# Kernel tuning notes

Measured on AMD Instinct MI355X. Metric: run time of the kernel, lower is better.

The kernel has to match this reference:

```python
import jax, jax.numpy as jnp
import numpy as np

DIM = 1024
NUM_HEADS = 16
HEAD_DIM = DIM // NUM_HEADS
B, S = 2, 2048


def setup_inputs() -> dict:
    key = jax.random.key(0)
    ks = jax.random.split(key, 7)
    x = jax.random.normal(ks[0], (B, S, DIM), dtype=jnp.float32)
    cos = jax.random.uniform(ks[1], (S, HEAD_DIM // 2), dtype=jnp.float32)
    sin = jax.random.uniform(ks[2], (S, HEAD_DIM // 2), dtype=jnp.float32)
    scale = 1.0 / np.sqrt(DIM)
    Wq = jax.random.normal(ks[3], (DIM, DIM), dtype=jnp.float32) * scale
    Wk = jax.random.normal(ks[4], (DIM, DIM), dtype=jnp.float32) * scale
    Wv = jax.random.normal(ks[5], (DIM, DIM), dtype=jnp.float32) * scale
    Wo = jax.random.normal(ks[6], (DIM, DIM), dtype=jnp.float32) * scale
    return {"x": x, "cos": cos, "sin": sin, "Wq": Wq, "Wk": Wk, "Wv": Wv, "Wo": Wo}


def _apply_rope(t, c, s):
    # t: [B, S, H, hd]; c, s: [1, S, 1, hd] (already doubled)
    half = t.shape[-1] // 2
    t1, t2 = t[..., :half], t[..., half:]
    rot = jnp.concatenate([-t2, t1], axis=-1)
    return t * c + rot * s


def reference(x, cos, sin, Wq, Wk, Wv, Wo):
    Bs, Ss, D = x.shape
    H, hd = NUM_HEADS, HEAD_DIM
    q = (x @ Wq).reshape(Bs, Ss, H, hd)
    k = (x @ Wk).reshape(Bs, Ss, H, hd)
    v = (x @ Wv).reshape(Bs, Ss, H, hd)
    # repeat(1,1,1,2) in torch tiles cos as [cos, cos] along last dim
    c = jnp.concatenate([cos, cos], axis=-1)[None, :, None, :]
    s = jnp.concatenate([sin, sin], axis=-1)[None, :, None, :]
    q = _apply_rope(q, c, s)
    k = _apply_rope(k, c, s)
    # SDPA, non-causal, scale 1/sqrt(hd)
    scores = jnp.einsum("bqhd,bkhd->bhqk", q, k) / jnp.sqrt(jnp.float32(hd))
    attn = jax.nn.softmax(scores, axis=-1)
    out = jnp.einsum("bhqk,bkhd->bqhd", attn, v).reshape(Bs, Ss, D)
    return out @ Wo
```

## Files before the change

### kernel.cpp

```cpp
#include <hip/hip_runtime.h>

#define B_  2
#define S_  2048
#define D_  1024
#define H_  16
#define HD_ 64
#define M_  (B_*S_)

typedef __bf16 bf16x8 __attribute__((ext_vector_type(8)));
typedef float  f32x4  __attribute__((ext_vector_type(4)));
typedef float  f32x16 __attribute__((ext_vector_type(16)));
typedef unsigned short ushort_t;

static __device__ __forceinline__ ushort_t f2bf(float f) {
  __bf16 b = (__bf16)f;
  return __builtin_bit_cast(ushort_t, b);
}

typedef __attribute__((address_space(1))) const unsigned u32g;
typedef __attribute__((address_space(3))) unsigned u32l;
static __device__ __forceinline__ void gll16(const ushort_t* g, __bf16* l) {
  __builtin_amdgcn_global_load_lds((u32g*)g, (u32l*)l, 16, 0, 0);
}

__global__ __launch_bounds__(256) void convert_x(const float* __restrict__ x,
                                                 ushort_t* __restrict__ xb) {
  size_t e = ((size_t)blockIdx.x * 256 + threadIdx.x) * 8;
  float4 a = *(const float4*)(x + e);
  float4 b = *(const float4*)(x + e + 4);
  uint4 pk;
  pk.x = (unsigned)f2bf(a.x) | ((unsigned)f2bf(a.y) << 16);
  pk.y = (unsigned)f2bf(a.z) | ((unsigned)f2bf(a.w) << 16);
  pk.z = (unsigned)f2bf(b.x) | ((unsigned)f2bf(b.y) << 16);
  pk.w = (unsigned)f2bf(b.z) | ((unsigned)f2bf(b.w) << 16);
  *(uint4*)(xb + e) = pk;
}

__global__ __launch_bounds__(256) void transpose_w(const float* __restrict__ Wq,
                                                   const float* __restrict__ Wk,
                                                   const float* __restrict__ Wv,
                                                   const float* __restrict__ Wo,
                                                   ushort_t* __restrict__ Wqkvt,
                                                   ushort_t* __restrict__ Wot) {
  __shared__ __bf16 T[64][72];
  const int z = blockIdx.z;
  const float* W = (z == 0) ? Wq : (z == 1) ? Wk : (z == 2) ? Wv : Wo;
  ushort_t* Wt = (z < 3) ? (Wqkvt + (size_t)z * 1048576) : Wot;
  const int k0 = blockIdx.y * 64, n0 = blockIdx.x * 64;
  const int t = threadIdx.x, r = t >> 2, c16 = (t & 3) * 16;
#pragma unroll
  for (int i = 0; i < 4; i++) {
    float4 v = *(const float4*)(W + (size_t)(k0 + r) * D_ + n0 + c16 + i * 4);
    T[r][c16 + i*4 + 0] = (__bf16)v.x;
    T[r][c16 + i*4 + 1] = (__bf16)v.y;
    T[r][c16 + i*4 + 2] = (__bf16)v.z;
    T[r][c16 + i*4 + 3] = (__bf16)v.w;
  }
  __syncthreads();
  ushort_t vals[16];
#pragma unroll
  for (int i = 0; i < 16; i++) vals[i] = __builtin_bit_cast(ushort_t, T[c16 + i][r]);
  ushort_t* dst = Wt + (size_t)(n0 + r) * D_ + k0 + c16;
  *(uint4*)dst       = *(const uint4*)&vals[0];
  *(uint4*)(dst + 8) = *(const uint4*)&vals[8];
}

__global__ __launch_bounds__(256) void transpose_v(const ushort_t* __restrict__ Vb,
                                                   ushort_t* __restrict__ Vtg) {
  __shared__ __bf16 T[64][72];
  const int bh = blockIdx.y, kt = blockIdx.x;
  const int t = threadIdx.x, r = t >> 2, c16 = (t & 3) * 16;
  const ushort_t* src = Vb + ((size_t)bh * S_ + kt*64 + r) * 64 + c16;
  *(uint4*)&T[r][c16]     = *(const uint4*)src;
  *(uint4*)&T[r][c16 + 8] = *(const uint4*)(src + 8);
  __syncthreads();
  ushort_t vals[16];
#pragma unroll
  for (int i = 0; i < 16; i++) {
    int c = c16 + i;
    int k = ((c & 1) << 5) | (c >> 1);
    vals[i] = __builtin_bit_cast(ushort_t, T[k][r]);
  }
  ushort_t* dst = Vtg + ((size_t)bh * 64 + r) * S_ + kt*64 + c16;
  *(uint4*)dst       = *(const uint4*)&vals[0];
  *(uint4*)(dst + 8) = *(const uint4*)&vals[8];
}

template<int OMODE>
__global__ __launch_bounds__(256) void gemm_bf16(const ushort_t* __restrict__ A,
                                                 const ushort_t* __restrict__ Bt,
                                                 void* __restrict__ Cp,
                                                 const float* __restrict__ cosb,
                                                 const float* __restrict__ sinb) {
  __shared__ __bf16 As[4096];
  __shared__ __bf16 Bs[4096];
  const int t = threadIdx.x, w = t >> 6, lane = t & 63, l15 = lane & 15, g = lane >> 4;
  const int wr = w >> 1, wc = w & 1;
  const int row0 = blockIdx.y * 128, col0 = blockIdx.x * 128;
  const int lr = t >> 2, lc = (t & 3) * 8;
  f32x4 acc[4][4] = {};

  for (int k0 = 0; k0 < D_; k0 += 32) {
    __syncthreads();
#pragma unroll
    for (int i = 0; i < 2; i++) {
      gll16(A  + (size_t)(row0 + i*64 + lr) * D_ + k0 + lc, &As[i*2048 + w*512]);
      gll16(Bt + (size_t)(col0 + i*64 + lr) * D_ + k0 + lc, &Bs[i*2048 + w*512]);
    }
    __syncthreads();
    bf16x8 af[4], bfv[4];
#pragma unroll
    for (int mt = 0; mt < 4; mt++) af[mt]  = *(const bf16x8*)&As[(wr*64 + mt*16 + l15)*32 + g*8];
#pragma unroll
    for (int nt = 0; nt < 4; nt++) bfv[nt] = *(const bf16x8*)&Bs[(wc*64 + nt*16 + l15)*32 + g*8];
#pragma unroll
    for (int mt = 0; mt < 4; mt++)
#pragma unroll
      for (int nt = 0; nt < 4; nt++)
        acc[mt][nt] = __builtin_amdgcn_mfma_f32_16x16x32_bf16(af[mt], bfv[nt], acc[mt][nt], 0, 0, 0);
  }

  if (OMODE == 0) {
#pragma unroll
    for (int mt = 0; mt < 4; mt++)
#pragma unroll
      for (int nt = 0; nt < 4; nt++) {
        int col = col0 + wc*64 + nt*16 + l15;
#pragma unroll
        for (int reg = 0; reg < 4; reg++) {
          int r = row0 + wr*64 + mt*16 + g*4 + reg;
          ((float*)Cp)[(size_t)r * D_ + col] = acc[mt][nt][reg];
        }
      }
  } else {
    const int mat = col0 >> 10;
    const int nc0 = (col0 + wc*64) & 1023;
    const int h = nc0 >> 6;
    ushort_t* dst = (ushort_t*)Cp + (size_t)mat * 4194304;
    const float QS = 0.125f * 1.4426950408889634f;
#pragma unroll
    for (int mt = 0; mt < 4; mt++) {
#pragma unroll
      for (int reg = 0; reg < 4; reg++) {
        int r = row0 + wr*64 + mt*16 + g*4 + reg;
        int b = r >> 11, s = r & (S_ - 1);
        size_t base = (((size_t)(b*H_ + h) * S_ + s) << 6);
        if (mat < 2) {
#pragma unroll
          for (int nt = 0; nt < 2; nt++) {
            int d1 = nt*16 + l15;
            float c  = cosb[s*32 + d1];
            float sn = sinb[s*32 + d1];
            float v1 = acc[mt][nt][reg], v2 = acc[mt][nt+2][reg];
            float r1 = v1*c - v2*sn;
            float r2 = v2*c + v1*sn;
            if (mat == 0) { r1 *= QS; r2 *= QS; }
            dst[base + d1]      = f2bf(r1);
            dst[base + d1 + 32] = f2bf(r2);
          }
        } else {
#pragma unroll
          for (int nt = 0; nt < 4; nt++)
            dst[base + nt*16 + l15] = f2bf(acc[mt][nt][reg]);
        }
      }
    }
  }
}

__global__ __launch_bounds__(256) void attn32(const ushort_t* __restrict__ Q,
                                              const ushort_t* __restrict__ K,
                                              const ushort_t* __restrict__ Vtg,
                                              ushort_t* __restrict__ Oa) {
  __shared__ __bf16 Ks[64][72];
  __shared__ __bf16 Vt[64][72];
  __shared__ __bf16 Ps[4][32][72];
  const int t = threadIdx.x, w = t >> 6, lane = t & 63;
  const int l31 = lane & 31, h2 = lane >> 5;
  const int bh = blockIdx.y, q0 = blockIdx.x * 128 + w * 32;

  const ushort_t* Qp = Q + ((size_t)bh * S_ + q0 + l31) * HD_;
  bf16x8 qf[4];
#pragma unroll
  for (int kc = 0; kc < 4; kc++) qf[kc] = *(const bf16x8*)(Qp + kc*16 + h2*8);

  f32x16 o0 = {}, o1 = {};
  float lp[16];
#pragma unroll
  for (int i = 0; i < 16; i++) lp[i] = 0.f;

  const ushort_t* Kb = K   + (size_t)bh * S_ * HD_;
  const ushort_t* Vg = Vtg + (size_t)bh * HD_ * S_;
  const int sr = t >> 3, sc8 = (t & 7) * 8;

  uint4 ka, kb, va, vb;
  {
    ka = *(const uint4*)(Kb + (size_t)(sr)      * HD_ + sc8);
    kb = *(const uint4*)(Kb + (size_t)(sr + 32) * HD_ + sc8);
    va = *(const uint4*)(Vg + (size_t)(sr)      * S_  + sc8);
    vb = *(const uint4*)(Vg + (size_t)(sr + 32) * S_  + sc8);
  }

  for (int kt = 0; kt < S_ / 64; kt++) {
    __syncthreads();
    *(uint4*)&Ks[sr][sc8]      = ka;
    *(uint4*)&Ks[sr + 32][sc8] = kb;
    *(uint4*)&Vt[sr][sc8]      = va;
    *(uint4*)&Vt[sr + 32][sc8] = vb;
    __syncthreads();
    if (kt < S_/64 - 1) {
      ka = *(const uint4*)(Kb + (size_t)((kt+1)*64 + sr)      * HD_ + sc8);
      kb = *(const uint4*)(Kb + (size_t)((kt+1)*64 + sr + 32) * HD_ + sc8);
      va = *(const uint4*)(Vg + (size_t)(sr)      * S_ + (kt+1)*64 + sc8);
      vb = *(const uint4*)(Vg + (size_t)(sr + 32) * S_ + (kt+1)*64 + sc8);
    }

    f32x16 s0 = {}, s1 = {};
#pragma unroll
    for (int kc = 0; kc < 4; kc++) {
      bf16x8 b0 = *(const bf16x8*)&Ks[l31][kc*16 + h2*8];
      bf16x8 b1 = *(const bf16x8*)&Ks[32 + l31][kc*16 + h2*8];
      s0 = __builtin_amdgcn_mfma_f32_32x32x16_bf16(qf[kc], b0, s0, 0, 0, 0);
      s1 = __builtin_amdgcn_mfma_f32_32x32x16_bf16(qf[kc], b1, s1, 0, 0, 0);
    }

#pragma unroll
    for (int i = 0; i < 16; i++) {
      float p0 = exp2f(s0[i]);
      float p1 = exp2f(s1[i]);
      lp[i] += p0 + p1;
      int row = (i & 3) + 8*(i >> 2) + 4*h2;
      unsigned pk = (unsigned)f2bf(p0) | ((unsigned)f2bf(p1) << 16);
      *(unsigned*)&Ps[w][row][2*l31] = pk;
    }

#pragma unroll
    for (int kc = 0; kc < 4; kc++) {
      bf16x8 pf = *(const bf16x8*)&Ps[w][l31][kc*16 + h2*8];
      bf16x8 v0 = *(const bf16x8*)&Vt[l31][kc*16 + h2*8];
      bf16x8 v1 = *(const bf16x8*)&Vt[32 + l31][kc*16 + h2*8];
      o0 = __builtin_amdgcn_mfma_f32_32x32x16_bf16(pf, v0, o0, 0, 0, 0);
      o1 = __builtin_amdgcn_mfma_f32_32x32x16_bf16(pf, v1, o1, 0, 0, 0);
    }
  }

#pragma unroll
  for (int i = 0; i < 16; i++) {
#pragma unroll
    for (int mk = 1; mk < 32; mk <<= 1) lp[i] += __shfl_xor(lp[i], mk, 64);
  }

  int b = bh >> 4, h = bh & 15;
#pragma unroll
  for (int i = 0; i < 16; i++) {
    float inv = 1.f / lp[i];
    int row = q0 + (i & 3) + 8*(i >> 2) + 4*h2;
    size_t base = (size_t)(b*S_ + row) * D_ + h*64;
    Oa[base + l31]      = f2bf(o0[i] * inv);
    Oa[base + 32 + l31] = f2bf(o1[i] * inv);
  }
}

extern "C" void kernel_launch(void* const* d_in, const int* in_sizes, int n_in,
                              void* d_out, int out_size, void* d_ws, size_t ws_size,
                              hipStream_t stream) {
  (void)in_sizes; (void)n_in; (void)out_size; (void)ws_size;
  const float* x    = (const float*)d_in[0];
  const float* cosb = (const float*)d_in[1];
  const float* sinb = (const float*)d_in[2];
  const float* Wq   = (const float*)d_in[3];
  const float* Wk   = (const float*)d_in[4];
  const float* Wv   = (const float*)d_in[5];
  const float* Wo   = (const float*)d_in[6];
  float* out = (float*)d_out;

  ushort_t* w     = (ushort_t*)d_ws;
  ushort_t* xb    = w;
  ushort_t* Wqkvt = w + 4194304;
  ushort_t* Wot   = w + 7340032;
  ushort_t* Qb    = w + 8388608;
  ushort_t* Kb    = w + 12582912;
  ushort_t* Vb    = w + 16777216;
  ushort_t* Vtg   = w + 20971520;
  ushort_t* att   = w + 25165824;

  convert_x<<<2048, 256, 0, stream>>>(x, xb);
  transpose_w<<<dim3(16, 16, 4), 256, 0, stream>>>(Wq, Wk, Wv, Wo, Wqkvt, Wot);

  gemm_bf16<1><<<dim3(24, 32), 256, 0, stream>>>(xb, Wqkvt, Qb, cosb, sinb);

  transpose_v<<<dim3(32, 32), 256, 0, stream>>>(Vb, Vtg);

  attn32<<<dim3(16, 32), 256, 0, stream>>>(Qb, Kb, Vtg, att);

  gemm_bf16<0><<<dim3(8, 32), 256, 0, stream>>>(att, Wot, out, nullptr, nullptr);
}
```

Before: 224.4 us.

## Split attention over key halves with combine pass; narrow output GEMM tiles

The attention kernel now splits the key/value sequence into two halves across a third grid dimension, writing unnormalized bf16 partial outputs and row sums into reused workspace buffers. A new combine kernel adds the partials and normalizes. The output projection GEMM is templated to a 64-wide N tile so it launches twice as many blocks. The aim is more blocks in flight to fill the GPU's compute units, at the cost of an extra kernel, extra memory traffic, and bf16 rounding of the partial sums. The split is only valid because the softmax has no max subtraction, so the two partials share a scale.

```diff
diff --git a/kernel.cpp b/kernel.cpp
--- a/kernel.cpp
+++ b/kernel.cpp
@@ -15,6 +15,9 @@
 static __device__ __forceinline__ ushort_t f2bf(float f) {
   __bf16 b = (__bf16)f;
   return __builtin_bit_cast(ushort_t, b);
+}
+static __device__ __forceinline__ float bf2f(ushort_t u) {
+  return (float)__builtin_bit_cast(__bf16, u);
 }
 
 typedef __attribute__((address_space(1))) const unsigned u32g;
@@ -86,37 +89,39 @@
   *(uint4*)(dst + 8) = *(const uint4*)&vals[8];
 }
 
-template<int OMODE>
+template<int OMODE, int BN>
 __global__ __launch_bounds__(256) void gemm_bf16(const ushort_t* __restrict__ A,
                                                  const ushort_t* __restrict__ Bt,
                                                  void* __restrict__ Cp,
                                                  const float* __restrict__ cosb,
                                                  const float* __restrict__ sinb) {
+  constexpr int NF = BN / 32;
   __shared__ __bf16 As[4096];
-  __shared__ __bf16 Bs[4096];
+  __shared__ __bf16 Bs[BN * 32];
   const int t = threadIdx.x, w = t >> 6, lane = t & 63, l15 = lane & 15, g = lane >> 4;
   const int wr = w >> 1, wc = w & 1;
-  const int row0 = blockIdx.y * 128, col0 = blockIdx.x * 128;
+  const int row0 = blockIdx.y * 128, col0 = blockIdx.x * BN;
   const int lr = t >> 2, lc = (t & 3) * 8;
-  f32x4 acc[4][4] = {};
+  f32x4 acc[4][NF] = {};
 
   for (int k0 = 0; k0 < D_; k0 += 32) {
     __syncthreads();
 #pragma unroll
-    for (int i = 0; i < 2; i++) {
-      gll16(A  + (size_t)(row0 + i*64 + lr) * D_ + k0 + lc, &As[i*2048 + w*512]);
+    for (int i = 0; i < 2; i++)
+      gll16(A + (size_t)(row0 + i*64 + lr) * D_ + k0 + lc, &As[i*2048 + w*512]);
+#pragma unroll
+    for (int i = 0; i < BN/64; i++)
       gll16(Bt + (size_t)(col0 + i*64 + lr) * D_ + k0 + lc, &Bs[i*2048 + w*512]);
-    }
     __syncthreads();
-    bf16x8 af[4], bfv[4];
-#pragma unroll
-    for (int mt = 0; mt < 4; mt++) af[mt]  = *(const bf16x8*)&As[(wr*64 + mt*16 + l15)*32 + g*8];
-#pragma unroll
-    for (int nt = 0; nt < 4; nt++) bfv[nt] = *(const bf16x8*)&Bs[(wc*64 + nt*16 + l15)*32 + g*8];
+    bf16x8 af[4], bfv[NF];
+#pragma unroll
+    for (int mt = 0; mt < 4; mt++)  af[mt]  = *(const bf16x8*)&As[(wr*64 + mt*16 + l15)*32 + g*8];
+#pragma unroll
+    for (int nt = 0; nt < NF; nt++) bfv[nt] = *(const bf16x8*)&Bs[(wc*(BN/2) + nt*16 + l15)*32 + g*8];
 #pragma unroll
     for (int mt = 0; mt < 4; mt++)
 #pragma unroll
-      for (int nt = 0; nt < 4; nt++)
+      for (int nt = 0; nt < NF; nt++)
         acc[mt][nt] = __builtin_amdgcn_mfma_f32_16x16x32_bf16(af[mt], bfv[nt], acc[mt][nt], 0, 0, 0);
   }
 
@@ -124,8 +129,8 @@
 #pragma unroll
     for (int mt = 0; mt < 4; mt++)
 #pragma unroll
-      for (int nt = 0; nt < 4; nt++) {
-        int col = col0 + wc*64 + nt*16 + l15;
+      for (int nt = 0; nt < NF; nt++) {
+        int col = col0 + wc*(BN/2) + nt*16 + l15;
 #pragma unroll
         for (int reg = 0; reg < 4; reg++) {
           int r = row0 + wr*64 + mt*16 + g*4 + reg;
@@ -171,13 +176,15 @@
 __global__ __launch_bounds__(256) void attn32(const ushort_t* __restrict__ Q,
                                               const ushort_t* __restrict__ K,
                                               const ushort_t* __restrict__ Vtg,
-                                              ushort_t* __restrict__ Oa) {
+                                              ushort_t* __restrict__ op0,
+                                              ushort_t* __restrict__ op1,
+                                              float* __restrict__ lw) {
   __shared__ __bf16 Ks[64][72];
   __shared__ __bf16 Vt[64][72];
   __shared__ __bf16 Ps[4][32][72];
   const int t = threadIdx.x, w = t >> 6, lane = t & 63;
   const int l31 = lane & 31, h2 = lane >> 5;
-  const int bh = blockIdx.y, q0 = blockIdx.x * 128 + w * 32;
+  const int bh = blockIdx.y, q0 = blockIdx.x * 128 + w * 32, z = blockIdx.z;
 
   const ushort_t* Qp = Q + ((size_t)bh * S_ + q0 + l31) * HD_;
   bf16x8 qf[4];
@@ -189,26 +196,24 @@
 #pragma unroll
   for (int i = 0; i < 16; i++) lp[i] = 0.f;
 
-  const ushort_t* Kb = K   + (size_t)bh * S_ * HD_;
-  const ushort_t* Vg = Vtg + (size_t)bh * HD_ * S_;
+  const ushort_t* Kb = K   + ((size_t)bh * S_ + z * 1024) * HD_;
+  const ushort_t* Vg = Vtg + (size_t)bh * HD_ * S_ + z * 1024;
   const int sr = t >> 3, sc8 = (t & 7) * 8;
 
   uint4 ka, kb, va, vb;
-  {
-    ka = *(const uint4*)(Kb + (size_t)(sr)      * HD_ + sc8);
-    kb = *(const uint4*)(Kb + (size_t)(sr + 32) * HD_ + sc8);
-    va = *(const uint4*)(Vg + (size_t)(sr)      * S_  + sc8);
-    vb = *(const uint4*)(Vg + (size_t)(sr + 32) * S_  + sc8);
-  }
-
-  for (int kt = 0; kt < S_ / 64; kt++) {
+  ka = *(const uint4*)(Kb + (size_t)(sr)      * HD_ + sc8);
+  kb = *(const uint4*)(Kb + (size_t)(sr + 32) * HD_ + sc8);
+  va = *(const uint4*)(Vg + (size_t)(sr)      * S_  + sc8);
+  vb = *(const uint4*)(Vg + (size_t)(sr + 32) * S_  + sc8);
+
+  for (int kt = 0; kt < 16; kt++) {
     __syncthreads();
     *(uint4*)&Ks[sr][sc8]      = ka;
     *(uint4*)&Ks[sr + 32][sc8] = kb;
     *(uint4*)&Vt[sr][sc8]      = va;
     *(uint4*)&Vt[sr + 32][sc8] = vb;
     __syncthreads();
-    if (kt < S_/64 - 1) {
+    if (kt < 15) {
       ka = *(const uint4*)(Kb + (size_t)((kt+1)*64 + sr)      * HD_ + sc8);
       kb = *(const uint4*)(Kb + (size_t)((kt+1)*64 + sr + 32) * HD_ + sc8);
       va = *(const uint4*)(Vg + (size_t)(sr)      * S_ + (kt+1)*64 + sc8);
@@ -250,15 +255,38 @@
     for (int mk = 1; mk < 32; mk <<= 1) lp[i] += __shfl_xor(lp[i], mk, 64);
   }
 
-  int b = bh >> 4, h = bh & 15;
+  ushort_t* op = (z == 0) ? op0 : op1;
+  float* lwp = lw + (size_t)(z*32 + bh) * S_;
 #pragma unroll
   for (int i = 0; i < 16; i++) {
-    float inv = 1.f / lp[i];
     int row = q0 + (i & 3) + 8*(i >> 2) + 4*h2;
-    size_t base = (size_t)(b*S_ + row) * D_ + h*64;
-    Oa[base + l31]      = f2bf(o0[i] * inv);
-    Oa[base + 32 + l31] = f2bf(o1[i] * inv);
-  }
+    size_t base = ((size_t)bh * S_ + row) * 64;
+    op[base + l31]      = f2bf(o0[i]);
+    op[base + 32 + l31] = f2bf(o1[i]);
+    if (l31 == 0) lwp[row] = lp[i];
+  }
+}
+
+__global__ __launch_bounds__(256) void combine(const ushort_t* __restrict__ op0,
+                                               const ushort_t* __restrict__ op1,
+                                               const float* __restrict__ lw,
+                                               ushort_t* __restrict__ att) {
+  int tid = blockIdx.x * 256 + threadIdx.x;
+  int d8 = (tid & 7) * 8;
+  int s  = (tid >> 3) & (S_ - 1);
+  int bh = tid >> 14;
+  size_t pb = ((size_t)bh * S_ + s) * 64 + d8;
+  uint4 a = *(const uint4*)(op0 + pb);
+  uint4 b = *(const uint4*)(op1 + pb);
+  float inv = 1.f / (lw[(size_t)bh * S_ + s] + lw[(size_t)(32 + bh) * S_ + s]);
+  const ushort_t* as = (const ushort_t*)&a;
+  const ushort_t* bs = (const ushort_t*)&b;
+  ushort_t outv[8];
+#pragma unroll
+  for (int i = 0; i < 8; i++)
+    outv[i] = f2bf((bf2f(as[i]) + bf2f(bs[i])) * inv);
+  int bidx = bh >> 4, h = bh & 15;
+  *(uint4*)(att + ((size_t)(bidx * S_ + s)) * D_ + h*64 + d8) = *(const uint4*)outv;
 }
 
 extern "C" void kernel_launch(void* const* d_in, const int* in_sizes, int n_in,
@@ -283,15 +311,18 @@
   ushort_t* Vb    = w + 16777216;
   ushort_t* Vtg   = w + 20971520;
   ushort_t* att   = w + 25165824;
+  float*    lw    = (float*)Wqkvt;
 
   convert_x<<<2048, 256, 0, stream>>>(x, xb);
   transpose_w<<<dim3(16, 16, 4), 256, 0, stream>>>(Wq, Wk, Wv, Wo, Wqkvt, Wot);
 
-  gemm_bf16<1><<<dim3(24, 32), 256, 0, stream>>>(xb, Wqkvt, Qb, cosb, sinb);
+  gemm_bf16<1,128><<<dim3(24, 32), 256, 0, stream>>>(xb, Wqkvt, Qb, cosb, sinb);
 
   transpose_v<<<dim3(32, 32), 256, 0, stream>>>(Vb, Vtg);
 
-  attn32<<<dim3(16, 32), 256, 0, stream>>>(Qb, Kb, Vtg, att);
-
-  gemm_bf16<0><<<dim3(8, 32), 256, 0, stream>>>(att, Wot, out, nullptr, nullptr);
-}
+  attn32<<<dim3(16, 32, 2), 256, 0, stream>>>(Qb, Kb, Vtg, xb, Vb, lw);
+
+  combine<<<2048, 256, 0, stream>>>(xb, Vb, lw, att);
+
+  gemm_bf16<0,64><<<dim3(16, 32), 256, 0, stream>>>(att, Wot, out, nullptr, nullptr);
+}
```

Result: no change. 224.8 us (+0.2%).
